# Optimization experiments

Hardware: AMD Instinct MI355X
Metric: run time of the kernel (lower is better)

## Reference

```python
import jax, jax.numpy as jnp
import numpy as np


def setup_inputs() -> dict:
    key = jax.random.key(0)
    k0, k1, k2, k3 = jax.random.split(key, 4)
    T, H, I, E, K = 2048, 2048, 1408, 8, 2  # tokens, hidden, intermediate, experts, top-k
    hidden_states = jax.random.normal(k0, (T, H), dtype=jnp.float32)
    router_weight = jax.random.normal(k1, (H, E), dtype=jnp.float32) * 0.02
    gate_up_weight = jax.random.normal(k2, (E, H, 2 * I), dtype=jnp.float32) * 0.02
    down_weight = jax.random.normal(k3, (E, I, H), dtype=jnp.float32) * 0.02
    return {
        "hidden_states": hidden_states,
        "router_weight": router_weight,
        "gate_up_weight": gate_up_weight,
        "down_weight": down_weight,
        "top_k": K,
    }


def reference(hidden_states, router_weight, gate_up_weight, down_weight, top_k):
    # Router: logits -> softmax -> top-k -> renormalize ('normalization' path)
    router_logits = hidden_states @ router_weight                  # [T, E]
    router_weights = jax.nn.softmax(router_logits, axis=-1)       # [T, E]
    topk_w, topk_idx = jax.lax.top_k(router_weights, top_k)       # [T, K]
    topk_w = topk_w / jnp.sum(topk_w, axis=-1, keepdims=True)     # router_weights_topk_reduced

    T, H = hidden_states.shape
    I = down_weight.shape[1]

    # Grouped gate_up GEMM (dense-per-expert reference for the grouped GMM)
    gate_up = jnp.einsum('th,ehf->etf', hidden_states, gate_up_weight)  # [E, T, 2I]
    gate, up = gate_up[..., :I], gate_up[..., I:]
    swish_out = jax.nn.silu(gate) * up                              # SWIGLU  [E, T, I]
    mlp_out = jnp.einsum('eti,eih->eth', swish_out, down_weight)    # [E, T, H]

    # Scatter-combine: gather each token's top-k expert outputs, weighted sum
    sel = mlp_out[topk_idx, jnp.arange(T)[:, None]]                 # [T, K, H]
    out = jnp.sum(sel * topk_w[..., None], axis=1)                  # [T, H]
    return out
```

## Files before the change

kernel.cpp:

```cpp
#include <hip/hip_runtime.h>
#include <hip/hip_bf16.h>
#include <math.h>

#define T_TOK 2048
#define HDIM  2048
#define IDIM  1408
#define NG    2816
#define NEXP  8
#define NPAIR (T_TOK*2)
#define RPAD  5120

typedef __attribute__((ext_vector_type(4))) float  f32x4;
typedef __attribute__((ext_vector_type(4))) short  s16x4;
typedef __attribute__((ext_vector_type(8))) short  s16x8;
typedef __attribute__((ext_vector_type(8))) __bf16 bf16x8;

__device__ __forceinline__ short f2bf(float f) {
  union { float f; unsigned u; } v; v.f = f;
  unsigned r = v.u + 0x7FFFu + ((v.u >> 16) & 1u);
  return (short)(r >> 16);
}

__device__ __forceinline__ void gload_lds16(const void* g, void* l) {
  __builtin_amdgcn_global_load_lds((const __attribute__((address_space(1))) unsigned int*)g,
                                   (__attribute__((address_space(3))) unsigned int*)l,
                                   16, 0, 0);
}

__device__ __forceinline__ void grid_remap(int orig, int NB, int* nb, int* rblk) {
  int wgid = (orig & 7) * (NB * 5) + (orig >> 3);
  int cid = wgid / (NB * 5), c = wgid % (NB * 5);
  int nbg = c / 10, rem = c % 10;
  *rblk = (rem >> 1) * 8 + cid;
  *nb = nbg * 2 + (rem & 1);
}

__global__ void router_kernel(const float* __restrict__ hs, const float* __restrict__ rw,
                              int* __restrict__ pair_e, float* __restrict__ pair_w,
                              int* __restrict__ pair_pos, int* __restrict__ counts) {
  int wid = threadIdx.x >> 6, lane = threadIdx.x & 63;
  int t = blockIdx.x * 4 + wid;
  float acc[NEXP];
#pragma unroll
  for (int e = 0; e < NEXP; e++) acc[e] = 0.f;
  const float* h = hs + (size_t)t * HDIM;
  for (int k = lane; k < HDIM; k += 64) {
    float x = h[k];
    f32x4 w0 = *(const f32x4*)(rw + (size_t)k * NEXP);
    f32x4 w1 = *(const f32x4*)(rw + (size_t)k * NEXP + 4);
#pragma unroll
    for (int e = 0; e < 4; e++) { acc[e] += x * w0[e]; acc[e + 4] += x * w1[e]; }
  }
#pragma unroll
  for (int e = 0; e < NEXP; e++)
#pragma unroll
    for (int off = 32; off > 0; off >>= 1)
      acc[e] += __shfl_xor(acc[e], off, 64);
  if (lane == 0) {
    int i1 = 0; float v1 = acc[0];
#pragma unroll
    for (int e = 1; e < NEXP; e++) if (acc[e] > v1) { v1 = acc[e]; i1 = e; }
    int i2 = -1; float v2 = -3.4e38f;
#pragma unroll
    for (int e = 0; e < NEXP; e++) if (e != i1 && acc[e] > v2) { v2 = acc[e]; i2 = e; }
    float w2 = 1.f / (1.f + expf(v1 - v2));
    float w1 = 1.f - w2;
    int p1 = atomicAdd(&counts[i1], 1);
    int p2 = atomicAdd(&counts[i2], 1);
    pair_e[2*t]   = i1; pair_w[2*t]   = w1; pair_pos[2*t]   = p1;
    pair_e[2*t+1] = i2; pair_w[2*t+1] = w2; pair_pos[2*t+1] = p2;
  }
}

__global__ void prefix_kernel(const int* __restrict__ counts, int* __restrict__ offs) {
  if (threadIdx.x == 0) {
    int s = 0;
    for (int e = 0; e < NEXP; e++) { offs[e] = s; s += (counts[e] + 127) & ~127; }
    offs[NEXP] = s;
  }
}

__global__ void rowmap_kernel(const int* __restrict__ pair_e, const float* __restrict__ pair_w,
                              const int* __restrict__ pair_pos, const int* __restrict__ offs,
                              int* __restrict__ row_token, float* __restrict__ row_weight) {
  int p = blockIdx.x * 256 + threadIdx.x;
  if (p >= NPAIR) return;
  int e = pair_e[p];
  int row = offs[e] + pair_pos[p];
  row_token[row] = p >> 1;
  row_weight[row] = pair_w[p];
}

__global__ __launch_bounds__(256) void gather_kernel(const float* __restrict__ hs,
                                                     const int* __restrict__ row_token,
                                                     short* __restrict__ A_c) {
  int r = blockIdx.x;
  int tok = row_token[r];
  int t = threadIdx.x;
  if (tok < 0) {
    *(s16x8*)&A_c[(size_t)r * HDIM + t * 8] = (s16x8)0;
    return;
  }
  const float* src = hs + (size_t)tok * HDIM + t * 8;
  f32x4 v0 = *(const f32x4*)src;
  f32x4 v1 = *(const f32x4*)(src + 4);
  s16x8 o;
#pragma unroll
  for (int j = 0; j < 4; j++) { o[j] = f2bf(v0[j]); o[4 + j] = f2bf(v1[j]); }
  int dstg = (t & ~7) | ((t & 7) ^ (r & 7));
  *(s16x8*)&A_c[(size_t)r * HDIM + dstg * 8] = o;
}

__global__ __launch_bounds__(256) void convert_w_kernel(
    const float* __restrict__ src, short* __restrict__ dst, int K, int N, int e_base) {
  int e = blockIdx.z + e_base;
  src += (size_t)e * K * N;
  dst += (size_t)blockIdx.z * K * N;
  int n0 = blockIdx.x * 64, k0 = blockIdx.y * 64;
  __shared__ short tile[64 * 76];
  int tid = threadIdx.x;
#pragma unroll
  for (int it = 0; it < 4; it++) {
    int s = tid + it * 256;
    int kk = s >> 4, nn = (s & 15) * 4;
    f32x4 v = *(const f32x4*)(src + (size_t)(k0 + kk) * N + n0 + nn);
    s16x4 b;
#pragma unroll
    for (int j = 0; j < 4; j++) b[j] = f2bf(v[j]);
    *(s16x4*)&tile[kk * 76 + nn] = b;
  }
  __syncthreads();
#pragma unroll
  for (int it = 0; it < 2; it++) {
    int s = tid + it * 256;
    int n = s >> 3, g = s & 7;
    int gs = g ^ (n & 7);
    s16x8 o;
#pragma unroll
    for (int j = 0; j < 8; j++) o[j] = tile[(gs * 8 + j) * 76 + n];
    *(s16x8*)&dst[(size_t)(n0 + n) * K + k0 + g * 8] = o;
  }
}

__global__ __launch_bounds__(256) void gateup_kernel(
    const short* __restrict__ A_c, const short* __restrict__ W,
    const int* __restrict__ offs, short* __restrict__ S,
    int e_only, size_t w_e_stride) {
  int orig = blockIdx.y * gridDim.x + blockIdx.x;
  int nb, rblk;
  grid_remap(orig, 22, &nb, &rblk);
  int rb = rblk * 128;
  if (rb >= offs[NEXP]) return;
  int e = 0;
#pragma unroll
  for (int i = 1; i < NEXP; i++) e += (rb >= offs[i]);
  if (e_only >= 0 && e != e_only) return;
  const short* Wb = W + (e_only >= 0 ? 0 : (size_t)e * w_e_stride);
  const short* Ar = A_c + (size_t)rb * HDIM;
  const short* Bg = Wb + (size_t)(nb * 64) * HDIM;
  const short* Bu = Wb + (size_t)(IDIM + nb * 64) * HDIM;

  __shared__ short As[2][128 * 64];
  __shared__ short Bgs[2][64 * 64];
  __shared__ short Bus[2][64 * 64];
  int tid = threadIdx.x, lane = tid & 63, wid = tid >> 6;
  int wm = wid >> 1, wn = wid & 1;
  int lm = lane & 15, lg = lane >> 4;

  f32x4 accg[4][2], accu[4][2];
#pragma unroll
  for (int a = 0; a < 4; a++)
#pragma unroll
    for (int b = 0; b < 2; b++) { accg[a][b] = (f32x4)0.f; accu[a][b] = (f32x4)0.f; }

  auto STAGE = [&](int buf, int kt) {
    int k0 = kt * 64;
#pragma unroll
    for (int it = 0; it < 4; it++) {
      int idx = tid + it * 256;
      gload_lds16(Ar + (size_t)(idx >> 3) * HDIM + k0 + (idx & 7) * 8, &As[buf][idx * 8]);
    }
#pragma unroll
    for (int it = 0; it < 2; it++) {
      int idx = tid + it * 256;
      gload_lds16(Bg + (size_t)(idx >> 3) * HDIM + k0 + (idx & 7) * 8, &Bgs[buf][idx * 8]);
      gload_lds16(Bu + (size_t)(idx >> 3) * HDIM + k0 + (idx & 7) * 8, &Bus[buf][idx * 8]);
    }
  };

  STAGE(0, 0);
  asm volatile("s_waitcnt vmcnt(0)" ::: "memory");
  __builtin_amdgcn_s_barrier();
  int cur = 0;
  for (int kt = 0; kt < HDIM / 64; kt++) {
    if (kt + 1 < HDIM / 64) STAGE(cur ^ 1, kt + 1);
    asm volatile("" ::: "memory");
#pragma unroll
    for (int ks = 0; ks < 2; ks++) {
      bf16x8 a[4], bg[2], bu[2];
#pragma unroll
      for (int mi = 0; mi < 4; mi++) {
        int m = wm * 64 + mi * 16 + lm;
        a[mi] = *(const bf16x8*)&As[cur][m * 64 + (((ks * 4 + lg) ^ (m & 7)) * 8)];
      }
#pragma unroll
      for (int nf = 0; nf < 2; nf++) {
        int n = wn * 32 + nf * 16 + lm;
        int off = n * 64 + (((ks * 4 + lg) ^ (n & 7)) * 8);
        bg[nf] = *(const bf16x8*)&Bgs[cur][off];
        bu[nf] = *(const bf16x8*)&Bus[cur][off];
      }
#pragma unroll
      for (int mi = 0; mi < 4; mi++)
#pragma unroll
        for (int nf = 0; nf < 2; nf++) {
          accg[mi][nf] = __builtin_amdgcn_mfma_f32_16x16x32_bf16(a[mi], bg[nf], accg[mi][nf], 0, 0, 0);
          accu[mi][nf] = __builtin_amdgcn_mfma_f32_16x16x32_bf16(a[mi], bu[nf], accu[mi][nf], 0, 0, 0);
        }
    }
    asm volatile("s_waitcnt vmcnt(0)" ::: "memory");
    __builtin_amdgcn_s_barrier();
    cur ^= 1;
  }
#pragma unroll
  for (int mi = 0; mi < 4; mi++)
#pragma unroll
    for (int nf = 0; nf < 2; nf++)
#pragma unroll
      for (int j = 0; j < 4; j++) {
        int row = wm * 64 + mi * 16 + lg * 4 + j;
        int rg = rb + row;
        int c6 = wn * 32 + nf * 16 + lm;
        int dc = (((c6 >> 3) ^ (rg & 7)) << 3) | (c6 & 7);
        float g = accg[mi][nf][j], u = accu[mi][nf][j];
        float sv = (g / (1.f + expf(-g))) * u;
        S[(size_t)rg * IDIM + nb * 64 + dc] = f2bf(sv);
      }
}

__global__ __launch_bounds__(256) void down_kernel(
    const short* __restrict__ S, const short* __restrict__ W,
    const int* __restrict__ offs, const int* __restrict__ row_token,
    const float* __restrict__ row_weight, float* __restrict__ out,
    int e_only, size_t w_e_stride) {
  int orig = blockIdx.y * gridDim.x + blockIdx.x;
  int nb, rblk;
  grid_remap(orig, 16, &nb, &rblk);
  int rb = rblk * 128;
  if (rb >= offs[NEXP]) return;
  int e = 0;
#pragma unroll
  for (int i = 1; i < NEXP; i++) e += (rb >= offs[i]);
  if (e_only >= 0 && e != e_only) return;
  const short* Ar = S + (size_t)rb * IDIM;
  const short* Bw = W + (e_only >= 0 ? 0 : (size_t)e * w_e_stride) + (size_t)(nb * 128) * IDIM;

  __shared__ short As[2][128 * 64];
  __shared__ short Bs[2][128 * 64];
  int tid = threadIdx.x, lane = tid & 63, wid = tid >> 6;
  int wm = wid >> 1, wn = wid & 1;
  int lm = lane & 15, lg = lane >> 4;

  f32x4 acc[4][4];
#pragma unroll
  for (int a = 0; a < 4; a++)
#pragma unroll
    for (int b = 0; b < 4; b++) acc[a][b] = (f32x4)0.f;

  auto STAGE = [&](int buf, int kt) {
    int k0 = kt * 64;
#pragma unroll
    for (int it = 0; it < 4; it++) {
      int idx = tid + it * 256;
      gload_lds16(Ar + (size_t)(idx >> 3) * IDIM + k0 + (idx & 7) * 8, &As[buf][idx * 8]);
      gload_lds16(Bw + (size_t)(idx >> 3) * IDIM + k0 + (idx & 7) * 8, &Bs[buf][idx * 8]);
    }
  };

  STAGE(0, 0);
  asm volatile("s_waitcnt vmcnt(0)" ::: "memory");
  __builtin_amdgcn_s_barrier();
  int cur = 0;
  for (int kt = 0; kt < IDIM / 64; kt++) {
    if (kt + 1 < IDIM / 64) STAGE(cur ^ 1, kt + 1);
    asm volatile("" ::: "memory");
#pragma unroll
    for (int ks = 0; ks < 2; ks++) {
      bf16x8 a[4], b[4];
#pragma unroll
      for (int mi = 0; mi < 4; mi++) {
        int m = wm * 64 + mi * 16 + lm;
        a[mi] = *(const bf16x8*)&As[cur][m * 64 + (((ks * 4 + lg) ^ (m & 7)) * 8)];
      }
#pragma unroll
      for (int nf = 0; nf < 4; nf++) {
        int n = wn * 64 + nf * 16 + lm;
        b[nf] = *(const bf16x8*)&Bs[cur][n * 64 + (((ks * 4 + lg) ^ (n & 7)) * 8)];
      }
#pragma unroll
      for (int mi = 0; mi < 4; mi++)
#pragma unroll
        for (int nf = 0; nf < 4; nf++)
          acc[mi][nf] = __builtin_amdgcn_mfma_f32_16x16x32_bf16(a[mi], b[nf], acc[mi][nf], 0, 0, 0);
    }
    asm volatile("s_waitcnt vmcnt(0)" ::: "memory");
    __builtin_amdgcn_s_barrier();
    cur ^= 1;
  }
#pragma unroll
  for (int mi = 0; mi < 4; mi++)
#pragma unroll
    for (int j = 0; j < 4; j++) {
      int row = wm * 64 + mi * 16 + lg * 4 + j;
      int tok = row_token[rb + row];
      if (tok >= 0) {
        float w = row_weight[rb + row];
#pragma unroll
        for (int nf = 0; nf < 4; nf++) {
          int col = nb * 128 + wn * 64 + nf * 16 + lm;
          atomicAdd(&out[(size_t)tok * HDIM + col], acc[mi][nf][j] * w);
        }
      }
    }
}

extern "C" void kernel_launch(void* const* d_in, const int* in_sizes, int n_in,
                              void* d_out, int out_size, void* d_ws, size_t ws_size,
                              hipStream_t stream) {
  const float* hs  = (const float*)d_in[0];
  const float* rw  = (const float*)d_in[1];
  const float* guw = (const float*)d_in[2];
  const float* dw  = (const float*)d_in[3];
  float* out = (float*)d_out;

  char* ws = (char*)d_ws;
  size_t off = 0;
  auto take = [&](size_t b) { size_t p = off; off = (off + b + 255) & ~(size_t)255; return p; };
  size_t s_off      = take((size_t)RPAD * IDIM * 2);
  int*   counts     = (int*)(ws + take(32 * 4));
  int*   offs       = (int*)(ws + take(16 * 4));
  int*   pair_e     = (int*)(ws + take(NPAIR * 4));
  float* pair_w     = (float*)(ws + take(NPAIR * 4));
  int*   pair_pos   = (int*)(ws + take(NPAIR * 4));
  int*   row_token  = (int*)(ws + take(RPAD * 4));
  float* row_weight = (float*)(ws + take(RPAD * 4));
  size_t ac_off  = take((size_t)RPAD * HDIM * 2);
  size_t wg_off  = off;

  short* S   = (short*)(ws + s_off);
  short* A_c = (short*)(ws + ac_off);

  const size_t WG_BYTES = (size_t)NEXP * NG * HDIM * 2;
  bool full = ws_size >= wg_off + WG_BYTES;

  hipMemsetAsync(counts, 0, 32 * 4, stream);
  hipMemsetAsync(row_token, 0xFF, RPAD * 4, stream);
  hipMemsetAsync(d_out, 0, (size_t)T_TOK * HDIM * 4, stream);

  router_kernel<<<T_TOK / 4, 256, 0, stream>>>(hs, rw, pair_e, pair_w, pair_pos, counts);
  prefix_kernel<<<1, 64, 0, stream>>>(counts, offs);
  rowmap_kernel<<<NPAIR / 256, 256, 0, stream>>>(pair_e, pair_w, pair_pos, offs,
                                                 row_token, row_weight);
  gather_kernel<<<RPAD, 256, 0, stream>>>(hs, row_token, A_c);

  if (full) {
    short* Wg = (short*)(ws + wg_off);
    short* Wd = (short*)(ws + ac_off);
    convert_w_kernel<<<dim3(NG / 64, HDIM / 64, NEXP), 256, 0, stream>>>(guw, Wg, HDIM, NG, 0);
    gateup_kernel<<<dim3(22, 40, 1), 256, 0, stream>>>(A_c, Wg, offs, S, -1, (size_t)NG * HDIM);
    convert_w_kernel<<<dim3(HDIM / 64, IDIM / 64, NEXP), 256, 0, stream>>>(dw, Wd, IDIM, HDIM, 0);
    down_kernel<<<dim3(16, 40, 1), 256, 0, stream>>>(S, Wd, offs, row_token, row_weight, out,
                                                     -1, (size_t)HDIM * IDIM);
  } else {
    short* slot = (short*)(ws + wg_off);
    for (int e = 0; e < NEXP; e++) {
      convert_w_kernel<<<dim3(NG / 64, HDIM / 64, 1), 256, 0, stream>>>(guw, slot, HDIM, NG, e);
      gateup_kernel<<<dim3(22, 40, 1), 256, 0, stream>>>(A_c, slot, offs, S, e, 0);
    }
    for (int e = 0; e < NEXP; e++) {
      convert_w_kernel<<<dim3(HDIM / 64, IDIM / 64, 1), 256, 0, stream>>>(dw, slot, IDIM, HDIM, e);
      down_kernel<<<dim3(16, 40, 1), 256, 0, stream>>>(S, slot, offs, row_token, row_weight, out, e, 0);
    }
  }
}
```

Before: 336.2 us.

## Replace atomic scatter with bf16 staging plus combine kernel; relax GEMM pipeline waits

The down GEMM now writes bf16 per-row outputs to a staging buffer instead of doing fp32 atomicAdds into the output, and a new combine kernel gathers each token's two expert rows and sums them with the router weights. This removes the output memset and the atomic traffic. Both GEMM main loops now wait with vmcnt(8) so the previous stage's loads can complete while the next stage's loads stay in flight. In exchange there is an extra kernel launch, an extra bf16 round trip of the expert outputs, and some rounding loss in the intermediate results.

```diff
diff --git a/kernel.cpp b/kernel.cpp
--- a/kernel.cpp
+++ b/kernel.cpp
@@ -21,6 +21,11 @@
   return (short)(r >> 16);
 }
 
+__device__ __forceinline__ float bf2f(short s) {
+  union { unsigned u; float f; } v; v.u = ((unsigned)(unsigned short)s) << 16;
+  return v.f;
+}
+
 __device__ __forceinline__ void gload_lds16(const void* g, void* l) {
   __builtin_amdgcn_global_load_lds((const __attribute__((address_space(1))) unsigned int*)g,
                                    (__attribute__((address_space(3))) unsigned int*)l,
@@ -82,13 +87,15 @@
 
 __global__ void rowmap_kernel(const int* __restrict__ pair_e, const float* __restrict__ pair_w,
                               const int* __restrict__ pair_pos, const int* __restrict__ offs,
-                              int* __restrict__ row_token, float* __restrict__ row_weight) {
+                              int* __restrict__ row_token, float* __restrict__ row_weight,
+                              int* __restrict__ tok2row) {
   int p = blockIdx.x * 256 + threadIdx.x;
   if (p >= NPAIR) return;
   int e = pair_e[p];
   int row = offs[e] + pair_pos[p];
   row_token[row] = p >> 1;
   row_weight[row] = pair_w[p];
+  tok2row[p] = row;
 }
 
 __global__ __launch_bounds__(256) void gather_kernel(const float* __restrict__ hs,
@@ -189,11 +196,16 @@
   };
 
   STAGE(0, 0);
-  asm volatile("s_waitcnt vmcnt(0)" ::: "memory");
-  __builtin_amdgcn_s_barrier();
   int cur = 0;
-  for (int kt = 0; kt < HDIM / 64; kt++) {
-    if (kt + 1 < HDIM / 64) STAGE(cur ^ 1, kt + 1);
+  const int NT = HDIM / 64;
+  for (int kt = 0; kt < NT; kt++) {
+    if (kt + 1 < NT) {
+      STAGE(cur ^ 1, kt + 1);
+      asm volatile("s_waitcnt vmcnt(8)" ::: "memory");
+    } else {
+      asm volatile("s_waitcnt vmcnt(0)" ::: "memory");
+    }
+    __builtin_amdgcn_s_barrier();
     asm volatile("" ::: "memory");
 #pragma unroll
     for (int ks = 0; ks < 2; ks++) {
@@ -218,7 +230,7 @@
           accu[mi][nf] = __builtin_amdgcn_mfma_f32_16x16x32_bf16(a[mi], bu[nf], accu[mi][nf], 0, 0, 0);
         }
     }
-    asm volatile("s_waitcnt vmcnt(0)" ::: "memory");
+    asm volatile("" ::: "memory");
     __builtin_amdgcn_s_barrier();
     cur ^= 1;
   }
@@ -240,8 +252,7 @@
 
 __global__ __launch_bounds__(256) void down_kernel(
     const short* __restrict__ S, const short* __restrict__ W,
-    const int* __restrict__ offs, const int* __restrict__ row_token,
-    const float* __restrict__ row_weight, float* __restrict__ out,
+    const int* __restrict__ offs, short* __restrict__ Sout,
     int e_only, size_t w_e_stride) {
   int orig = blockIdx.y * gridDim.x + blockIdx.x;
   int nb, rblk;
@@ -278,11 +289,16 @@
   };
 
   STAGE(0, 0);
-  asm volatile("s_waitcnt vmcnt(0)" ::: "memory");
-  __builtin_amdgcn_s_barrier();
   int cur = 0;
-  for (int kt = 0; kt < IDIM / 64; kt++) {
-    if (kt + 1 < IDIM / 64) STAGE(cur ^ 1, kt + 1);
+  const int NT = IDIM / 64;
+  for (int kt = 0; kt < NT; kt++) {
+    if (kt + 1 < NT) {
+      STAGE(cur ^ 1, kt + 1);
+      asm volatile("s_waitcnt vmcnt(8)" ::: "memory");
+    } else {
+      asm volatile("s_waitcnt vmcnt(0)" ::: "memory");
+    }
+    __builtin_amdgcn_s_barrier();
     asm volatile("" ::: "memory");
 #pragma unroll
     for (int ks = 0; ks < 2; ks++) {
@@ -303,7 +319,7 @@
         for (int nf = 0; nf < 4; nf++)
           acc[mi][nf] = __builtin_amdgcn_mfma_f32_16x16x32_bf16(a[mi], b[nf], acc[mi][nf], 0, 0, 0);
     }
-    asm volatile("s_waitcnt vmcnt(0)" ::: "memory");
+    asm volatile("" ::: "memory");
     __builtin_amdgcn_s_barrier();
     cur ^= 1;
   }
@@ -312,16 +328,26 @@
 #pragma unroll
     for (int j = 0; j < 4; j++) {
       int row = wm * 64 + mi * 16 + lg * 4 + j;
-      int tok = row_token[rb + row];
-      if (tok >= 0) {
-        float w = row_weight[rb + row];
-#pragma unroll
-        for (int nf = 0; nf < 4; nf++) {
-          int col = nb * 128 + wn * 64 + nf * 16 + lm;
-          atomicAdd(&out[(size_t)tok * HDIM + col], acc[mi][nf][j] * w);
-        }
-      }
-    }
+#pragma unroll
+      for (int nf = 0; nf < 4; nf++) {
+        int col = nb * 128 + wn * 64 + nf * 16 + lm;
+        Sout[(size_t)(rb + row) * HDIM + col] = f2bf(acc[mi][nf][j]);
+      }
+    }
+}
+
+__global__ __launch_bounds__(256) void combine_kernel(
+    const short* __restrict__ Sout, const int* __restrict__ tok2row,
+    const float* __restrict__ row_weight, float* __restrict__ out) {
+  int t = blockIdx.x;
+  int r1 = tok2row[2 * t], r2 = tok2row[2 * t + 1];
+  float w1 = row_weight[r1], w2 = row_weight[r2];
+  int c = threadIdx.x * 8;
+  s16x8 a = *(const s16x8*)&Sout[(size_t)r1 * HDIM + c];
+  s16x8 b = *(const s16x8*)&Sout[(size_t)r2 * HDIM + c];
+  float* o = out + (size_t)t * HDIM + c;
+#pragma unroll
+  for (int j = 0; j < 8; j++) o[j] = w1 * bf2f(a[j]) + w2 * bf2f(b[j]);
 }
 
 extern "C" void kernel_launch(void* const* d_in, const int* in_sizes, int n_in,
@@ -344,6 +370,7 @@
   int*   pair_pos   = (int*)(ws + take(NPAIR * 4));
   int*   row_token  = (int*)(ws + take(RPAD * 4));
   float* row_weight = (float*)(ws + take(RPAD * 4));
+  int*   tok2row    = (int*)(ws + take(NPAIR * 4));
   size_t ac_off  = take((size_t)RPAD * HDIM * 2);
   size_t wg_off  = off;
 
@@ -351,35 +378,39 @@
   short* A_c = (short*)(ws + ac_off);
 
   const size_t WG_BYTES = (size_t)NEXP * NG * HDIM * 2;
+  const size_t WD_BYTES = (size_t)NEXP * HDIM * IDIM * 2;
   bool full = ws_size >= wg_off + WG_BYTES;
 
   hipMemsetAsync(counts, 0, 32 * 4, stream);
   hipMemsetAsync(row_token, 0xFF, RPAD * 4, stream);
-  hipMemsetAsync(d_out, 0, (size_t)T_TOK * HDIM * 4, stream);
 
   router_kernel<<<T_TOK / 4, 256, 0, stream>>>(hs, rw, pair_e, pair_w, pair_pos, counts);
   prefix_kernel<<<1, 64, 0, stream>>>(counts, offs);
   rowmap_kernel<<<NPAIR / 256, 256, 0, stream>>>(pair_e, pair_w, pair_pos, offs,
-                                                 row_token, row_weight);
+                                                 row_token, row_weight, tok2row);
   gather_kernel<<<RPAD, 256, 0, stream>>>(hs, row_token, A_c);
 
   if (full) {
-    short* Wg = (short*)(ws + wg_off);
-    short* Wd = (short*)(ws + ac_off);
+    short* Wg   = (short*)(ws + wg_off);
+    short* Wd   = (short*)(ws + ac_off);
+    short* Sout = (short*)(ws + ac_off + ((size_t)48 << 20));
     convert_w_kernel<<<dim3(NG / 64, HDIM / 64, NEXP), 256, 0, stream>>>(guw, Wg, HDIM, NG, 0);
     gateup_kernel<<<dim3(22, 40, 1), 256, 0, stream>>>(A_c, Wg, offs, S, -1, (size_t)NG * HDIM);
     convert_w_kernel<<<dim3(HDIM / 64, IDIM / 64, NEXP), 256, 0, stream>>>(dw, Wd, IDIM, HDIM, 0);
-    down_kernel<<<dim3(16, 40, 1), 256, 0, stream>>>(S, Wd, offs, row_token, row_weight, out,
-                                                     -1, (size_t)HDIM * IDIM);
+    down_kernel<<<dim3(16, 40, 1), 256, 0, stream>>>(S, Wd, offs, Sout, -1, (size_t)HDIM * IDIM);
+    combine_kernel<<<T_TOK, 256, 0, stream>>>(Sout, tok2row, row_weight, out);
   } else {
     short* slot = (short*)(ws + wg_off);
+    short* Sout = (short*)(ws + wg_off + ((size_t)12 << 20));
+    (void)WD_BYTES;
     for (int e = 0; e < NEXP; e++) {
       convert_w_kernel<<<dim3(NG / 64, HDIM / 64, 1), 256, 0, stream>>>(guw, slot, HDIM, NG, e);
       gateup_kernel<<<dim3(22, 40, 1), 256, 0, stream>>>(A_c, slot, offs, S, e, 0);
     }
     for (int e = 0; e < NEXP; e++) {
       convert_w_kernel<<<dim3(HDIM / 64, IDIM / 64, 1), 256, 0, stream>>>(dw, slot, IDIM, HDIM, e);
-      down_kernel<<<dim3(16, 40, 1), 256, 0, stream>>>(S, slot, offs, row_token, row_weight, out, e, 0);
-    }
-  }
-}
+      down_kernel<<<dim3(16, 40, 1), 256, 0, stream>>>(S, slot, offs, Sout, e, 0);
+    }
+    combine_kernel<<<T_TOK, 256, 0, stream>>>(Sout, tok2row, row_weight, out);
+  }
+}
```

After: 310.8 us. 1.08x faster.
